# Kernel tuning notes

Hardware: AMD Instinct MI355X
Metric: run time of the kernel (lower is better)

Reference implementation:

```python
import jax, jax.numpy as jnp
import numpy as np
from functools import partial

B, R, C = 32, 300, 37            # frames, rois/frame, classes (incl. background)
SCORE_THR, NMS_THR = 0.1, 0.4    # thresholds from the source
BBOX_STD = jnp.array([0.1, 0.1, 0.2, 0.2], dtype=jnp.float32)
IMG_H, IMG_W, IMG_SCALE = 1067.0, 600.0, 1.6667


def setup_inputs() -> dict:
    key = jax.random.key(0)
    k1, k2, k3, k4, k5, k6 = jax.random.split(key, 6)
    # plausible RPN proposals inside the (scaled) image
    cx = jax.random.uniform(k1, (B, R)) * (IMG_W - 1.0)
    cy = jax.random.uniform(k2, (B, R)) * (IMG_H - 1.0)
    w = jax.random.uniform(k3, (B, R)) * 200.0 + 20.0
    h = jax.random.uniform(k4, (B, R)) * 200.0 + 20.0
    rois_boxes = jnp.stack([
        jnp.clip(cx - 0.5 * w, 0.0, IMG_W - 1.0),
        jnp.clip(cy - 0.5 * h, 0.0, IMG_H - 1.0),
        jnp.clip(cx + 0.5 * w, 0.0, IMG_W - 1.0),
        jnp.clip(cy + 0.5 * h, 0.0, IMG_H - 1.0)], axis=-1).astype(jnp.float32)
    bbox_pred = (jax.random.normal(k5, (B, R, 4 * C)) * 0.5).astype(jnp.float32)
    scores = jax.nn.softmax(jax.random.normal(k6, (B, R, C)) * 2.0, axis=-1).astype(jnp.float32)
    im_info = jnp.tile(jnp.array([IMG_H, IMG_W, IMG_SCALE], dtype=jnp.float32), (B, 1))
    return {"rois_boxes": rois_boxes, "bbox_pred": bbox_pred,
            "scores": scores, "im_info": im_info}


def _pairwise_iou(b):  # b: [R,4] -> [R,R], torchvision convention (no +1)
    area = (b[:, 2] - b[:, 0]) * (b[:, 3] - b[:, 1])
    lt = jnp.maximum(b[:, None, :2], b[None, :, :2])
    rb = jnp.minimum(b[:, None, 2:], b[None, :, 2:])
    wh = jnp.clip(rb - lt, 0.0)
    inter = wh[..., 0] * wh[..., 1]
    return inter / (area[:, None] + area[None, :] - inter + 1e-12)


def _nms_keep(boxes, scores):  # boxes [R,4], scores [R] -> bool keep mask [R]
    order = jnp.argsort(-scores)
    b, s = boxes[order], scores[order]
    iou = _pairwise_iou(b)                    # [R,R]
    idx = jnp.arange(R)
    valid = s > SCORE_THR

    def body(i, keep):
        sup = keep[i] & (iou[i] > NMS_THR) & (idx > i)
        return keep & ~sup

    keep_sorted = jax.lax.fori_loop(0, R, body, valid)
    return jnp.zeros(R, dtype=bool).at[order].set(keep_sorted)


def reference(rois_boxes, bbox_pred, scores, im_info):
    deltas = bbox_pred.reshape(B, R, C, 4) * BBOX_STD          # un-normalize
    x1, y1, x2, y2 = [rois_boxes[..., k] for k in range(4)]    # each [B,R]
    w = x2 - x1 + 1.0
    h = y2 - y1 + 1.0
    cx = x1 + 0.5 * w
    cy = y1 + 0.5 * h
    dx, dy, dw, dh = [deltas[..., k] for k in range(4)]        # each [B,R,C]
    pcx = dx * w[..., None] + cx[..., None]
    pcy = dy * h[..., None] + cy[..., None]
    pw = jnp.exp(dw) * w[..., None]
    ph = jnp.exp(dh) * h[..., None]
    px1 = pcx - 0.5 * pw
    py1 = pcy - 0.5 * ph
    px2 = pcx + 0.5 * pw
    py2 = pcy + 0.5 * ph
    # ---- clip_boxes to per-image (H, W) in scaled coords ----
    Wm1 = im_info[:, 1][:, None, None] - 1.0
    Hm1 = im_info[:, 0][:, None, None] - 1.0
    px1 = jnp.clip(px1, 0.0, Wm1)
    py1 = jnp.clip(py1, 0.0, Hm1)
    px2 = jnp.clip(px2, 0.0, Wm1)
    py2 = jnp.clip(py2, 0.0, Hm1)
    boxes = jnp.stack([px1, py1, px2, py2], axis=-1) / im_info[0, 2]  # [B,R,C,4]

    # ---- per-image, per-class NMS (classes 1..C-1, background skipped) ----
    cls_boxes = jnp.transpose(boxes[:, :, 1:, :], (0, 2, 1, 3))   # [B,C-1,R,4]
    cls_scores = jnp.transpose(scores[:, :, 1:], (0, 2, 1))       # [B,C-1,R]
    keep = jax.vmap(jax.vmap(_nms_keep))(cls_boxes, cls_scores)   # [B,C-1,R] bool

    # person class (j==1 -> slice index 0): keep only the single top detection
    sc0, k0 = cls_scores[:, 0, :], keep[:, 0, :]
    any0 = jnp.any(k0, axis=-1)
    top0 = jnp.argmax(jnp.where(k0, sc0, -jnp.inf), axis=-1)
    oh = (jnp.arange(R)[None, :] == top0[:, None]) & any0[:, None]
    keep = keep.at[:, 0, :].set(oh)

    # padded cls_dets: [B, C-1, R, 5], zeros where suppressed
    dets = jnp.concatenate([cls_boxes, cls_scores[..., None]], axis=-1)
    dets = jnp.clip(dets, 0.0) * keep[..., None].astype(dets.dtype)
    return dets
```

## Files before the change

### kernel.cpp

```cpp
#include <hip/hip_runtime.h>

#define RR 300
#define NCLS 37
#define COUT 36
#define NSTRIP 5
#define CAP2 128
#define SCORE_THR_C 0.1f
#define NMS_THR_C 0.4f

__device__ __forceinline__ float readlanef(float x, int sl) {
    return __uint_as_float((unsigned)__builtin_amdgcn_readlane((int)__float_as_uint(x), sl));
}

__global__ __launch_bounds__(64) void det_wave4_kernel(
    const float* __restrict__ rois,
    const float* __restrict__ pred,
    const float* __restrict__ scr,
    const float* __restrict__ iminfo,
    float* __restrict__ out)
{
#pragma clang fp contract(off)
    const int bid  = blockIdx.x;
    const int lane = threadIdx.x;
    const int bc   = (bid & 7) * 144 + (bid >> 3);
    const int b    = bc / COUT;
    const int c    = bc % COUT;
    const int cls  = c + 1;

    __shared__ __align__(16) float csc[CAP2 + 4];
    __shared__ int          cro[CAP2];
    __shared__ float4       sbx[CAP2];
    __shared__ int          sor[CAP2];
    __shared__ float4       vals4[RR];
    __shared__ unsigned int kpz[80];

    unsigned char* kp = (unsigned char*)kpz;
    kpz[lane] = 0u;
    if (lane < 16) kpz[64 + lane] = 0u;

    float ss[NSTRIP];
    bool  vv[NSTRIP];
    #pragma unroll
    for (int t = 0; t < NSTRIP; ++t) {
        const int r = lane + 64 * t;
        ss[t] = (r < RR) ? scr[(size_t)(b * RR + r) * NCLS + cls] : 0.f;
        vv[t] = (r < RR) && (ss[t] > SCORE_THR_C);
    }

    const unsigned long long lmask = (1ull << lane) - 1ull;
    int pos[NSTRIP];
    int acc = 0;
    #pragma unroll
    for (int t = 0; t < NSTRIP; ++t) {
        const unsigned long long balt = __ballot(vv[t]);
        pos[t] = acc + __popcll(balt & lmask);
        acc   += __popcll(balt);
    }
    int nv = __builtin_amdgcn_readfirstlane(acc);
    if (nv > CAP2) nv = CAP2;

    #pragma unroll
    for (int t = 0; t < NSTRIP; ++t) {
        if (vv[t] && pos[t] < CAP2) {
            csc[pos[t]] = ss[t];
            cro[pos[t]] = lane + 64 * t;
        }
    }
    if (lane < 4) csc[nv + lane] = -1.0f;

    const float Hm1 = iminfo[b * 3 + 0] - 1.0f;
    const float Wm1 = iminfo[b * 3 + 1] - 1.0f;
    const float scl = iminfo[2];

    const bool has2 = (nv > 64);
    const bool a0 = (lane < nv);
    const bool a1 = has2 && (lane + 64 < nv);

    float  s0 = -2.f, s1 = -2.f;
    int    o0 = 0, o1 = 0;
    float4 b0 = make_float4(0.f, 0.f, 0.f, 0.f), b1 = b0;
    if (a0) {
        s0 = csc[lane];
        o0 = cro[lane];
        const float4 ro = *reinterpret_cast<const float4*>(rois + (size_t)(b * RR + o0) * 4);
        const float4 pp = *reinterpret_cast<const float4*>(pred + (size_t)(b * RR + o0) * (4 * NCLS) + 4 * cls);
        float w  = ro.z - ro.x + 1.0f;
        float h  = ro.w - ro.y + 1.0f;
        float cx = ro.x + 0.5f * w;
        float cy = ro.y + 0.5f * h;
        float dx = pp.x * 0.1f;
        float dy = pp.y * 0.1f;
        float dw = pp.z * 0.2f;
        float dh = pp.w * 0.2f;
        float pcx = dx * w + cx;
        float pcy = dy * h + cy;
        float pw  = expf(dw) * w;
        float ph  = expf(dh) * h;
        b0.x = fminf(fmaxf(pcx - 0.5f * pw, 0.0f), Wm1) / scl;
        b0.y = fminf(fmaxf(pcy - 0.5f * ph, 0.0f), Hm1) / scl;
        b0.z = fminf(fmaxf(pcx + 0.5f * pw, 0.0f), Wm1) / scl;
        b0.w = fminf(fmaxf(pcy + 0.5f * ph, 0.0f), Hm1) / scl;
    }
    if (a1) {
        s1 = csc[lane + 64];
        o1 = cro[lane + 64];
        const float4 ro = *reinterpret_cast<const float4*>(rois + (size_t)(b * RR + o1) * 4);
        const float4 pp = *reinterpret_cast<const float4*>(pred + (size_t)(b * RR + o1) * (4 * NCLS) + 4 * cls);
        float w  = ro.z - ro.x + 1.0f;
        float h  = ro.w - ro.y + 1.0f;
        float cx = ro.x + 0.5f * w;
        float cy = ro.y + 0.5f * h;
        float dx = pp.x * 0.1f;
        float dy = pp.y * 0.1f;
        float dw = pp.z * 0.2f;
        float dh = pp.w * 0.2f;
        float pcx = dx * w + cx;
        float pcy = dy * h + cy;
        float pw  = expf(dw) * w;
        float ph  = expf(dh) * h;
        b1.x = fminf(fmaxf(pcx - 0.5f * pw, 0.0f), Wm1) / scl;
        b1.y = fminf(fmaxf(pcy - 0.5f * ph, 0.0f), Hm1) / scl;
        b1.z = fminf(fmaxf(pcx + 0.5f * pw, 0.0f), Wm1) / scl;
        b1.w = fminf(fmaxf(pcy + 0.5f * ph, 0.0f), Hm1) / scl;
    }

    int r0 = 0, r1 = 0;
    const float4* cs4 = reinterpret_cast<const float4*>(&csc[0]);
    const int n4 = (nv + 3) >> 2;
    for (int q4 = 0; q4 < n4; ++q4) {
        const float4 sv = cs4[q4];
        const int qb = q4 * 4;
        r0 += (int)(sv.x > s0) + ((int)(sv.x == s0) & (int)(qb + 0 < lane));
        r0 += (int)(sv.y > s0) + ((int)(sv.y == s0) & (int)(qb + 1 < lane));
        r0 += (int)(sv.z > s0) + ((int)(sv.z == s0) & (int)(qb + 2 < lane));
        r0 += (int)(sv.w > s0) + ((int)(sv.w == s0) & (int)(qb + 3 < lane));
    }
    if (has2) {
        for (int q4 = 0; q4 < n4; ++q4) {
            const float4 sv = cs4[q4];
            const int qb = q4 * 4, me = lane + 64;
            r1 += (int)(sv.x > s1) + ((int)(sv.x == s1) & (int)(qb + 0 < me));
            r1 += (int)(sv.y > s1) + ((int)(sv.y == s1) & (int)(qb + 1 < me));
            r1 += (int)(sv.z > s1) + ((int)(sv.z == s1) & (int)(qb + 2 < me));
            r1 += (int)(sv.w > s1) + ((int)(sv.w == s1) & (int)(qb + 3 < me));
        }
    }

    if (a0) { sbx[r0] = b0; sor[r0] = o0; }
    if (a1) { sbx[r1] = b1; sor[r1] = o1; }
    float4 sb0 = make_float4(0.f, 0.f, 0.f, 0.f), sb1 = sb0;
    float  sa0 = 0.f, sa1 = 0.f;
    int    so0 = 0, so1 = 0;
    if (a0) { sb0 = sbx[lane];      so0 = sor[lane];
              sa0 = (sb0.z - sb0.x) * (sb0.w - sb0.y); }
    if (a1) { sb1 = sbx[lane + 64]; so1 = sor[lane + 64];
              sa1 = (sb1.z - sb1.x) * (sb1.w - sb1.y); }

    unsigned long long lv0, lv1, kb0 = 0ull, kb1 = 0ull;
    lv0 = (nv >= 64) ? ~0ull : ((1ull << nv) - 1ull);
    lv1 = has2 ? ((nv >= 128) ? ~0ull : ((1ull << (nv - 64)) - 1ull)) : 0ull;
    int top_orig = -1;
    for (;;) {
        int p;
        if (lv0)      p = __builtin_ctzll(lv0);
        else if (lv1) p = 64 + __builtin_ctzll(lv1);
        else          break;
        const int sp = __builtin_amdgcn_readfirstlane(p);

        float px1, py1, px2, py2;
        int   po;
        if (sp < 64) {
            px1 = readlanef(sb0.x, sp); py1 = readlanef(sb0.y, sp);
            px2 = readlanef(sb0.z, sp); py2 = readlanef(sb0.w, sp);
            po  = __builtin_amdgcn_readlane(so0, sp);
            kb0 |= 1ull << sp;  lv0 &= ~(1ull << sp);
        } else {
            const int sq = sp - 64;
            px1 = readlanef(sb1.x, sq); py1 = readlanef(sb1.y, sq);
            px2 = readlanef(sb1.z, sq); py2 = readlanef(sb1.w, sq);
            po  = __builtin_amdgcn_readlane(so1, sq);
            kb1 |= 1ull << sq;  lv1 &= ~(1ull << sq);
        }
        if (top_orig < 0) top_orig = po;
        const float pa = (px2 - px1) * (py2 - py1);

        {
            float lx = fmaxf(px1, sb0.x);
            float ly = fmaxf(py1, sb0.y);
            float rx = fminf(px2, sb0.z);
            float ry = fminf(py2, sb0.w);
            float iw = fmaxf(rx - lx, 0.0f);
            float ih = fmaxf(ry - ly, 0.0f);
            float inter = iw * ih;
            float den = pa + sa0 - inter + 1e-12f;
            float iou = inter / den;
            lv0 &= ~__ballot(a0 && (lane > sp) && (iou > NMS_THR_C));
        }
        if (has2) {
            float lx = fmaxf(px1, sb1.x);
            float ly = fmaxf(py1, sb1.y);
            float rx = fminf(px2, sb1.z);
            float ry = fminf(py2, sb1.w);
            float iw = fmaxf(rx - lx, 0.0f);
            float ih = fmaxf(ry - ly, 0.0f);
            float inter = iw * ih;
            float den = pa + sa1 - inter + 1e-12f;
            float iou = inter / den;
            lv1 &= ~__ballot(a1 && (lane + 64 > sp) && (iou > NMS_THR_C));
        }
    }

    if (a0 && ((kb0 >> lane) & 1ull)) { vals4[so0] = sb0; kp[so0] = 1; }
    if (a1 && ((kb1 >> lane) & 1ull)) { vals4[so1] = sb1; kp[so1] = 1; }

    #pragma unroll
    for (int t = 0; t < NSTRIP; ++t) {
        const int r = lane + 64 * t;
        if (r < RR) {
            const bool k = (c == 0) ? (r == top_orig) : (kp[r] != 0);
            float q0 = 0.f, q1 = 0.f, q2 = 0.f, q3 = 0.f, q4 = 0.f;
            if (k) {
                const float4 v4 = vals4[r];
                q0 = fmaxf(v4.x, 0.0f);
                q1 = fmaxf(v4.y, 0.0f);
                q2 = fmaxf(v4.z, 0.0f);
                q3 = fmaxf(v4.w, 0.0f);
                q4 = fmaxf(ss[t], 0.0f);
            }
            const size_t base = (((size_t)b * COUT + c) * RR + r) * 5;
            out[base + 0] = q0;
            out[base + 1] = q1;
            out[base + 2] = q2;
            out[base + 3] = q3;
            out[base + 4] = q4;
        }
    }
}

extern "C" void kernel_launch(void* const* d_in, const int* in_sizes, int n_in,
                              void* d_out, int out_size, void* d_ws, size_t ws_size,
                              hipStream_t stream) {
    const float* rois   = (const float*)d_in[0];
    const float* pred   = (const float*)d_in[1];
    const float* scores = (const float*)d_in[2];
    const float* iminfo = (const float*)d_in[3];
    float* out = (float*)d_out;
    det_wave4_kernel<<<dim3(1152), dim3(64), 0, stream>>>(rois, pred, scores, iminfo, out);
}
```

Baseline: 18.63 us.

## Precompute suppression bitmask matrix then resolve NMS with cheap ballot loop

Replaces the serial greedy NMS loop, which read each pivot box through readlanes and computed IoU against all lanes per kept box, with a two-phase scheme. First every lane computes its IoU against all candidates and builds per-lane bitmasks of which higher-ranked boxes suppress it. A short serial loop then resolves keep status using only bit tests and ballots. Kept rows are written straight from registers, and only the suppressed rows get zeros, which removes the vals4 LDS staging. The cost is IoU work for all nv×nv pairs instead of only the kept pivots, plus a divergent per-bit shift into 64-bit masks.

After: 19.28 us. 1.03x slower.

```diff
diff --git a/kernel.cpp b/kernel.cpp
--- a/kernel.cpp
+++ b/kernel.cpp
@@ -8,11 +8,11 @@
 #define SCORE_THR_C 0.1f
 #define NMS_THR_C 0.4f
 
-__device__ __forceinline__ float readlanef(float x, int sl) {
-    return __uint_as_float((unsigned)__builtin_amdgcn_readlane((int)__float_as_uint(x), sl));
+__device__ __forceinline__ int readlanei(int x, int sl) {
+    return __builtin_amdgcn_readlane(x, sl);
 }
 
-__global__ __launch_bounds__(64) void det_wave4_kernel(
+__global__ __launch_bounds__(64) void det_wave5_kernel(
     const float* __restrict__ rois,
     const float* __restrict__ pred,
     const float* __restrict__ scr,
@@ -31,7 +31,7 @@
     __shared__ int          cro[CAP2];
     __shared__ float4       sbx[CAP2];
     __shared__ int          sor[CAP2];
-    __shared__ float4       vals4[RR];
+    __shared__ float        ssc[CAP2];
     __shared__ unsigned int kpz[80];
 
     unsigned char* kp = (unsigned char*)kpz;
@@ -146,93 +146,104 @@
         }
     }
 
-    if (a0) { sbx[r0] = b0; sor[r0] = o0; }
-    if (a1) { sbx[r1] = b1; sor[r1] = o1; }
+    if (a0) { sbx[r0] = b0; sor[r0] = o0; ssc[r0] = s0; }
+    if (a1) { sbx[r1] = b1; sor[r1] = o1; ssc[r1] = s1; }
     float4 sb0 = make_float4(0.f, 0.f, 0.f, 0.f), sb1 = sb0;
-    float  sa0 = 0.f, sa1 = 0.f;
+    float  sa0 = 0.f, sa1 = 0.f, sc0 = 0.f, sc1 = 0.f;
     int    so0 = 0, so1 = 0;
-    if (a0) { sb0 = sbx[lane];      so0 = sor[lane];
+    if (a0) { sb0 = sbx[lane];      so0 = sor[lane];      sc0 = ssc[lane];
               sa0 = (sb0.z - sb0.x) * (sb0.w - sb0.y); }
-    if (a1) { sb1 = sbx[lane + 64]; so1 = sor[lane + 64];
+    if (a1) { sb1 = sbx[lane + 64]; so1 = sor[lane + 64]; sc1 = ssc[lane + 64];
               sa1 = (sb1.z - sb1.x) * (sb1.w - sb1.y); }
 
-    unsigned long long lv0, lv1, kb0 = 0ull, kb1 = 0ull;
-    lv0 = (nv >= 64) ? ~0ull : ((1ull << nv) - 1ull);
-    lv1 = has2 ? ((nv >= 128) ? ~0ull : ((1ull << (nv - 64)) - 1ull)) : 0ull;
-    int top_orig = -1;
-    for (;;) {
-        int p;
-        if (lv0)      p = __builtin_ctzll(lv0);
-        else if (lv1) p = 64 + __builtin_ctzll(lv1);
-        else          break;
-        const int sp = __builtin_amdgcn_readfirstlane(p);
-
-        float px1, py1, px2, py2;
-        int   po;
-        if (sp < 64) {
-            px1 = readlanef(sb0.x, sp); py1 = readlanef(sb0.y, sp);
-            px2 = readlanef(sb0.z, sp); py2 = readlanef(sb0.w, sp);
-            po  = __builtin_amdgcn_readlane(so0, sp);
-            kb0 |= 1ull << sp;  lv0 &= ~(1ull << sp);
-        } else {
-            const int sq = sp - 64;
-            px1 = readlanef(sb1.x, sq); py1 = readlanef(sb1.y, sq);
-            px2 = readlanef(sb1.z, sq); py2 = readlanef(sb1.w, sq);
-            po  = __builtin_amdgcn_readlane(so1, sq);
-            kb1 |= 1ull << sq;  lv1 &= ~(1ull << sq);
-        }
-        if (top_orig < 0) top_orig = po;
-        const float pa = (px2 - px1) * (py2 - py1);
-
+    unsigned long long cAlo = 0ull, cAhi = 0ull, cBlo = 0ull, cBhi = 0ull;
+    for (int q = 0; q < nv; ++q) {
+        const float4 bq = sbx[q];
+        const float  aq = (bq.z - bq.x) * (bq.w - bq.y);
         {
-            float lx = fmaxf(px1, sb0.x);
-            float ly = fmaxf(py1, sb0.y);
-            float rx = fminf(px2, sb0.z);
-            float ry = fminf(py2, sb0.w);
+            float lx = fmaxf(bq.x, sb0.x);
+            float ly = fmaxf(bq.y, sb0.y);
+            float rx = fminf(bq.z, sb0.z);
+            float ry = fminf(bq.w, sb0.w);
             float iw = fmaxf(rx - lx, 0.0f);
             float ih = fmaxf(ry - ly, 0.0f);
             float inter = iw * ih;
-            float den = pa + sa0 - inter + 1e-12f;
+            float den = aq + sa0 - inter + 1e-12f;
             float iou = inter / den;
-            lv0 &= ~__ballot(a0 && (lane > sp) && (iou > NMS_THR_C));
+            const bool s = a0 && (q < lane) && (iou > NMS_THR_C);
+            if (q < 64) cAlo |= ((unsigned long long)s) << q;
+            else        cAhi |= ((unsigned long long)s) << (q - 64);
         }
         if (has2) {
-            float lx = fmaxf(px1, sb1.x);
-            float ly = fmaxf(py1, sb1.y);
-            float rx = fminf(px2, sb1.z);
-            float ry = fminf(py2, sb1.w);
+            float lx = fmaxf(bq.x, sb1.x);
+            float ly = fmaxf(bq.y, sb1.y);
+            float rx = fminf(bq.z, sb1.z);
+            float ry = fminf(bq.w, sb1.w);
             float iw = fmaxf(rx - lx, 0.0f);
             float ih = fmaxf(ry - ly, 0.0f);
             float inter = iw * ih;
-            float den = pa + sa1 - inter + 1e-12f;
+            float den = aq + sa1 - inter + 1e-12f;
             float iou = inter / den;
-            lv1 &= ~__ballot(a1 && (lane + 64 > sp) && (iou > NMS_THR_C));
-        }
-    }
-
-    if (a0 && ((kb0 >> lane) & 1ull)) { vals4[so0] = sb0; kp[so0] = 1; }
-    if (a1 && ((kb1 >> lane) & 1ull)) { vals4[so1] = sb1; kp[so1] = 1; }
+            const bool s = a1 && (q < lane + 64) && (iou > NMS_THR_C);
+            if (q < 64) cBlo |= ((unsigned long long)s) << q;
+            else        cBhi |= ((unsigned long long)s) << (q - 64);
+        }
+    }
+
+    unsigned long long live0 = (nv >= 64) ? ~0ull : ((1ull << nv) - 1ull);
+    unsigned long long live1 = has2 ? ((nv >= 128) ? ~0ull : ((1ull << (nv - 64)) - 1ull)) : 0ull;
+    unsigned long long k0 = 0ull, k1 = 0ull;
+    while (live0 | live1) {
+        if (live0) {
+            const int sp = __builtin_ctzll(live0);
+            k0 |= 1ull << sp;
+            live0 &= ~(1ull << sp);
+            live0 &= ~__ballot(((cAlo >> sp) & 1ull) != 0ull);
+            if (has2) live1 &= ~__ballot(((cBlo >> sp) & 1ull) != 0ull);
+        } else {
+            const int sp = __builtin_ctzll(live1);
+            k1 |= 1ull << sp;
+            live1 &= ~(1ull << sp);
+            live1 &= ~__ballot(((cBhi >> sp) & 1ull) != 0ull);
+        }
+    }
+
+    const bool kept0 = a0 && ((k0 >> lane) & 1ull);
+    const bool kept1 = a1 && ((k1 >> lane) & 1ull);
+    if (kept0) kp[so0] = 1;
+    if (kept1) kp[so1] = 1;
+    const int top_orig = (nv > 0) ? readlanei(so0, 0) : -1;
+
+    if (kept0 && (c != 0 || lane == 0)) {
+        const size_t base = (((size_t)b * COUT + c) * RR + so0) * 5;
+        out[base + 0] = fmaxf(sb0.x, 0.0f);
+        out[base + 1] = fmaxf(sb0.y, 0.0f);
+        out[base + 2] = fmaxf(sb0.z, 0.0f);
+        out[base + 3] = fmaxf(sb0.w, 0.0f);
+        out[base + 4] = fmaxf(sc0,   0.0f);
+    }
+    if (kept1 && (c != 0)) {
+        const size_t base = (((size_t)b * COUT + c) * RR + so1) * 5;
+        out[base + 0] = fmaxf(sb1.x, 0.0f);
+        out[base + 1] = fmaxf(sb1.y, 0.0f);
+        out[base + 2] = fmaxf(sb1.z, 0.0f);
+        out[base + 3] = fmaxf(sb1.w, 0.0f);
+        out[base + 4] = fmaxf(sc1,   0.0f);
+    }
 
     #pragma unroll
     for (int t = 0; t < NSTRIP; ++t) {
         const int r = lane + 64 * t;
         if (r < RR) {
-            const bool k = (c == 0) ? (r == top_orig) : (kp[r] != 0);
-            float q0 = 0.f, q1 = 0.f, q2 = 0.f, q3 = 0.f, q4 = 0.f;
-            if (k) {
-                const float4 v4 = vals4[r];
-                q0 = fmaxf(v4.x, 0.0f);
-                q1 = fmaxf(v4.y, 0.0f);
-                q2 = fmaxf(v4.z, 0.0f);
-                q3 = fmaxf(v4.w, 0.0f);
-                q4 = fmaxf(ss[t], 0.0f);
+            const bool keeprow = (c == 0) ? (r == top_orig) : (kp[r] != 0);
+            if (!keeprow) {
+                const size_t base = (((size_t)b * COUT + c) * RR + r) * 5;
+                out[base + 0] = 0.0f;
+                out[base + 1] = 0.0f;
+                out[base + 2] = 0.0f;
+                out[base + 3] = 0.0f;
+                out[base + 4] = 0.0f;
             }
-            const size_t base = (((size_t)b * COUT + c) * RR + r) * 5;
-            out[base + 0] = q0;
-            out[base + 1] = q1;
-            out[base + 2] = q2;
-            out[base + 3] = q3;
-            out[base + 4] = q4;
         }
     }
 }
@@ -245,5 +256,5 @@
     const float* scores = (const float*)d_in[2];
     const float* iminfo = (const float*)d_in[3];
     float* out = (float*)d_out;
-    det_wave4_kernel<<<dim3(1152), dim3(64), 0, stream>>>(rois, pred, scores, iminfo, out);
+    det_wave5_kernel<<<dim3(1152), dim3(64), 0, stream>>>(rois, pred, scores, iminfo, out);
 }
```

## Stage output tile in LDS for float4 stores and prefetch rois/pred coalesced

Applied to the files above, without the earlier changes.

The output for each (image, class) block is now assembled in a 1500-float shared buffer, zeroed up front, and written to global memory with contiguous float4 stores instead of five strided scalar stores per roi. All 300 rois and class deltas are prefetched into shared memory with coalesced loads, replacing the dependent gather of only the valid candidates. The person-class top-1 handling now keeps sorted lane 0 directly instead of tracking the original index. In exchange it loads more data up front and uses more shared memory per block, which may lower occupancy.

After: 19.79 us. +6.2%, slower.

```diff
diff --git a/kernel.cpp b/kernel.cpp
--- a/kernel.cpp
+++ b/kernel.cpp
@@ -11,8 +11,11 @@
 __device__ __forceinline__ float readlanef(float x, int sl) {
     return __uint_as_float((unsigned)__builtin_amdgcn_readlane((int)__float_as_uint(x), sl));
 }
-
-__global__ __launch_bounds__(64) void det_wave4_kernel(
+__device__ __forceinline__ int readlanei(int x, int sl) {
+    return __builtin_amdgcn_readlane(x, sl);
+}
+
+__global__ __launch_bounds__(64) void det_wave6_kernel(
     const float* __restrict__ rois,
     const float* __restrict__ pred,
     const float* __restrict__ scr,
@@ -27,24 +30,36 @@
     const int c    = bc % COUT;
     const int cls  = c + 1;
 
-    __shared__ __align__(16) float csc[CAP2 + 4];
+    __shared__ __align__(16) float4 Lro[RR];
+    __shared__ __align__(16) float4 Lpp[RR];
+    __shared__ __align__(16) float  csc[CAP2 + 4];
     __shared__ int          cro[CAP2];
-    __shared__ float4       sbx[CAP2];
+    __shared__ __align__(16) float4 sbx[CAP2];
     __shared__ int          sor[CAP2];
-    __shared__ float4       vals4[RR];
-    __shared__ unsigned int kpz[80];
-
-    unsigned char* kp = (unsigned char*)kpz;
-    kpz[lane] = 0u;
-    if (lane < 16) kpz[64 + lane] = 0u;
+    __shared__ float        ssc[CAP2];
+    __shared__ __align__(16) float obuf[1500];
 
     float ss[NSTRIP];
     bool  vv[NSTRIP];
     #pragma unroll
     for (int t = 0; t < NSTRIP; ++t) {
         const int r = lane + 64 * t;
-        ss[t] = (r < RR) ? scr[(size_t)(b * RR + r) * NCLS + cls] : 0.f;
-        vv[t] = (r < RR) && (ss[t] > SCORE_THR_C);
+        if (r < RR) {
+            const float4 ro = *reinterpret_cast<const float4*>(rois + (size_t)(b * RR + r) * 4);
+            const float4 pp = *reinterpret_cast<const float4*>(pred + (size_t)(b * RR + r) * (4 * NCLS) + 4 * cls);
+            ss[t] = scr[(size_t)(b * RR + r) * NCLS + cls];
+            Lro[r] = ro;
+            Lpp[r] = pp;
+        } else {
+            ss[t] = 0.f;
+        }
+        vv[t] = (lane + 64 * t < RR) && (ss[t] > SCORE_THR_C);
+    }
+    float4* ob4 = reinterpret_cast<float4*>(obuf);
+    #pragma unroll
+    for (int k = 0; k < 6; ++k) {
+        const int i = lane + 64 * k;
+        if (i < 375) ob4[i] = make_float4(0.f, 0.f, 0.f, 0.f);
     }
 
     const unsigned long long lmask = (1ull << lane) - 1ull;
@@ -82,8 +97,8 @@
     if (a0) {
         s0 = csc[lane];
         o0 = cro[lane];
-        const float4 ro = *reinterpret_cast<const float4*>(rois + (size_t)(b * RR + o0) * 4);
-        const float4 pp = *reinterpret_cast<const float4*>(pred + (size_t)(b * RR + o0) * (4 * NCLS) + 4 * cls);
+        const float4 ro = Lro[o0];
+        const float4 pp = Lpp[o0];
         float w  = ro.z - ro.x + 1.0f;
         float h  = ro.w - ro.y + 1.0f;
         float cx = ro.x + 0.5f * w;
@@ -104,8 +119,8 @@
     if (a1) {
         s1 = csc[lane + 64];
         o1 = cro[lane + 64];
-        const float4 ro = *reinterpret_cast<const float4*>(rois + (size_t)(b * RR + o1) * 4);
-        const float4 pp = *reinterpret_cast<const float4*>(pred + (size_t)(b * RR + o1) * (4 * NCLS) + 4 * cls);
+        const float4 ro = Lro[o1];
+        const float4 pp = Lpp[o1];
         float w  = ro.z - ro.x + 1.0f;
         float h  = ro.w - ro.y + 1.0f;
         float cx = ro.x + 0.5f * w;
@@ -146,20 +161,19 @@
         }
     }
 
-    if (a0) { sbx[r0] = b0; sor[r0] = o0; }
-    if (a1) { sbx[r1] = b1; sor[r1] = o1; }
+    if (a0) { sbx[r0] = b0; sor[r0] = o0; ssc[r0] = s0; }
+    if (a1) { sbx[r1] = b1; sor[r1] = o1; ssc[r1] = s1; }
     float4 sb0 = make_float4(0.f, 0.f, 0.f, 0.f), sb1 = sb0;
-    float  sa0 = 0.f, sa1 = 0.f;
+    float  sa0 = 0.f, sa1 = 0.f, sc0 = 0.f, sc1 = 0.f;
     int    so0 = 0, so1 = 0;
-    if (a0) { sb0 = sbx[lane];      so0 = sor[lane];
+    if (a0) { sb0 = sbx[lane];      so0 = sor[lane];      sc0 = ssc[lane];
               sa0 = (sb0.z - sb0.x) * (sb0.w - sb0.y); }
-    if (a1) { sb1 = sbx[lane + 64]; so1 = sor[lane + 64];
+    if (a1) { sb1 = sbx[lane + 64]; so1 = sor[lane + 64]; sc1 = ssc[lane + 64];
               sa1 = (sb1.z - sb1.x) * (sb1.w - sb1.y); }
 
     unsigned long long lv0, lv1, kb0 = 0ull, kb1 = 0ull;
     lv0 = (nv >= 64) ? ~0ull : ((1ull << nv) - 1ull);
     lv1 = has2 ? ((nv >= 128) ? ~0ull : ((1ull << (nv - 64)) - 1ull)) : 0ull;
-    int top_orig = -1;
     for (;;) {
         int p;
         if (lv0)      p = __builtin_ctzll(lv0);
@@ -168,20 +182,16 @@
         const int sp = __builtin_amdgcn_readfirstlane(p);
 
         float px1, py1, px2, py2;
-        int   po;
         if (sp < 64) {
             px1 = readlanef(sb0.x, sp); py1 = readlanef(sb0.y, sp);
             px2 = readlanef(sb0.z, sp); py2 = readlanef(sb0.w, sp);
-            po  = __builtin_amdgcn_readlane(so0, sp);
             kb0 |= 1ull << sp;  lv0 &= ~(1ull << sp);
         } else {
             const int sq = sp - 64;
             px1 = readlanef(sb1.x, sq); py1 = readlanef(sb1.y, sq);
             px2 = readlanef(sb1.z, sq); py2 = readlanef(sb1.w, sq);
-            po  = __builtin_amdgcn_readlane(so1, sq);
             kb1 |= 1ull << sq;  lv1 &= ~(1ull << sq);
         }
-        if (top_orig < 0) top_orig = po;
         const float pa = (px2 - px1) * (py2 - py1);
 
         {
@@ -210,29 +220,32 @@
         }
     }
 
-    if (a0 && ((kb0 >> lane) & 1ull)) { vals4[so0] = sb0; kp[so0] = 1; }
-    if (a1 && ((kb1 >> lane) & 1ull)) { vals4[so1] = sb1; kp[so1] = 1; }
-
-    #pragma unroll
-    for (int t = 0; t < NSTRIP; ++t) {
-        const int r = lane + 64 * t;
-        if (r < RR) {
-            const bool k = (c == 0) ? (r == top_orig) : (kp[r] != 0);
-            float q0 = 0.f, q1 = 0.f, q2 = 0.f, q3 = 0.f, q4 = 0.f;
-            if (k) {
-                const float4 v4 = vals4[r];
-                q0 = fmaxf(v4.x, 0.0f);
-                q1 = fmaxf(v4.y, 0.0f);
-                q2 = fmaxf(v4.z, 0.0f);
-                q3 = fmaxf(v4.w, 0.0f);
-                q4 = fmaxf(ss[t], 0.0f);
-            }
-            const size_t base = (((size_t)b * COUT + c) * RR + r) * 5;
-            out[base + 0] = q0;
-            out[base + 1] = q1;
-            out[base + 2] = q2;
-            out[base + 3] = q3;
-            out[base + 4] = q4;
+    const bool kept0 = a0 && ((kb0 >> lane) & 1ull) && (c != 0 || lane == 0);
+    const bool kept1 = a1 && ((kb1 >> lane) & 1ull) && (c != 0);
+    if (kept0) {
+        const int base = so0 * 5;
+        obuf[base + 0] = fmaxf(sb0.x, 0.0f);
+        obuf[base + 1] = fmaxf(sb0.y, 0.0f);
+        obuf[base + 2] = fmaxf(sb0.z, 0.0f);
+        obuf[base + 3] = fmaxf(sb0.w, 0.0f);
+        obuf[base + 4] = fmaxf(sc0,   0.0f);
+    }
+    if (kept1) {
+        const int base = so1 * 5;
+        obuf[base + 0] = fmaxf(sb1.x, 0.0f);
+        obuf[base + 1] = fmaxf(sb1.y, 0.0f);
+        obuf[base + 2] = fmaxf(sb1.z, 0.0f);
+        obuf[base + 3] = fmaxf(sb1.w, 0.0f);
+        obuf[base + 4] = fmaxf(sc1,   0.0f);
+    }
+
+    float* outbc = out + (size_t)bc * 1500;
+    #pragma unroll
+    for (int k = 0; k < 6; ++k) {
+        const int i = lane + 64 * k;
+        if (i < 375) {
+            const float4 v = ob4[i];
+            *reinterpret_cast<float4*>(outbc + 4 * i) = v;
         }
     }
 }
@@ -245,5 +258,5 @@
     const float* scores = (const float*)d_in[2];
     const float* iminfo = (const float*)d_in[3];
     float* out = (float*)d_out;
-    det_wave4_kernel<<<dim3(1152), dim3(64), 0, stream>>>(rois, pred, scores, iminfo, out);
-}
+    det_wave6_kernel<<<dim3(1152), dim3(64), 0, stream>>>(rois, pred, scores, iminfo, out);
+}
```
